# Kernel tuning notes

Measured on AMD Instinct MI355X. Metric: run time of the kernel, lower is better.

The kernel has to match this reference:

```python
import jax, jax.numpy as jnp
import numpy as np

NEG = -1e20
EPS = float(np.finfo(np.float32).eps)


def setup_inputs() -> dict:
    key = jax.random.key(0)
    k1, k2, k3, k4 = jax.random.split(key, 4)
    B, S, E, D = 8, 2048, 1024, 1024
    return {
        "embeddings": jax.random.normal(k1, (B, S, E), dtype=jnp.float32),
        "mask": jnp.ones((B, S), dtype=jnp.int32),
        "W_q": jax.random.normal(k2, (E, D), dtype=jnp.float32),
        "W_k": jax.random.normal(k3, (E, D), dtype=jnp.float32),
        "W_v": jax.random.normal(k4, (E, D), dtype=jnp.float32),
    }


def reference(embeddings, mask, W_q, W_k, W_v):
    # embeddings: [B,S,E]; mask: [B,S] (1 = keep, 0 = pad)
    q = embeddings @ W_q            # [B,S,D]
    k = embeddings @ W_k            # [B,S,D]
    v = embeddings @ W_v            # [B,S,Dv]
    energy = jnp.einsum("bqd,bkd->bqk", q, k)  # [B,S,S]
    S = embeddings.shape[1]
    causal = jnp.tril(jnp.ones((S, S), dtype=bool))          # [S,S]
    energy = jnp.where(causal[None, :, :], energy, NEG)
    pad = (mask == 0)[:, None, :]                             # [B,1,S]
    energy = jnp.where(pad, NEG, energy)
    d_k = jnp.float32(W_k.shape[1])
    scale = jnp.sqrt(d_k) + EPS
    attention = jax.nn.softmax(energy / scale, axis=-1)       # [B,S,S]
    output = jnp.einsum("bqk,bkd->bqd", attention, v)         # [B,S,Dv]
    return output, attention
```

## Files before the change

kernel.cpp:

```cpp
#include <hip/hip_runtime.h>

#define Bb 8
#define Ss 2048
#define Ee 1024
#define Dd 1024

typedef __attribute__((ext_vector_type(8))) __bf16 bf16x8;
typedef __attribute__((ext_vector_type(4))) float f32x4;
typedef unsigned short u16;

__device__ __forceinline__ u16 f2bf(float x) {
  unsigned u = __float_as_uint(x);
  return (u16)((u + 0x7fffu + ((u >> 16) & 1u)) >> 16);
}
__device__ __forceinline__ float bf2f(u16 h) {
  return __uint_as_float(((unsigned)h) << 16);
}

__device__ __forceinline__ void gload16(const void* g, void* l) {
  __builtin_amdgcn_global_load_lds(
      (__attribute__((address_space(1))) void*)const_cast<void*>(g),
      (__attribute__((address_space(3))) void*)l, 16, 0, 0);
}

#define MFMA_BF16 __builtin_amdgcn_mfma_f32_16x16x32_bf16

__global__ __launch_bounds__(256) void k_split4(const float* __restrict__ in,
                                                u16* __restrict__ hi,
                                                u16* __restrict__ lo,
                                                long long n4) {
  long long i = (long long)blockIdx.x * 256 + threadIdx.x;
  if (i >= n4) return;
  float4 v = ((const float4*)in)[i];
  float xs[4] = {v.x, v.y, v.z, v.w};
  u16 hh[4], ll[4];
#pragma unroll
  for (int j = 0; j < 4; ++j) {
    hh[j] = f2bf(xs[j]);
    ll[j] = f2bf(xs[j] - bf2f(hh[j]));
  }
  ushort4 h, l;
  h.x = hh[0]; h.y = hh[1]; h.z = hh[2]; h.w = hh[3];
  l.x = ll[0]; l.y = ll[1]; l.z = ll[2]; l.w = ll[3];
  ((ushort4*)hi)[i] = h;
  ((ushort4*)lo)[i] = l;
}

__global__ __launch_bounds__(256) void k_wt_split(const float* __restrict__ W,
                                                  u16* __restrict__ hi,
                                                  u16* __restrict__ lo) {
  __shared__ float t[32][33];
  const int tx = threadIdx.x & 31;
  const int ty = threadIdx.x >> 5;
  const int e0 = blockIdx.y * 32, d0 = blockIdx.x * 32;
#pragma unroll
  for (int r = ty; r < 32; r += 8)
    t[r][tx] = W[(long long)(e0 + r) * Dd + d0 + tx];
  __syncthreads();
#pragma unroll
  for (int r = ty; r < 32; r += 8) {
    float x = t[tx][r];
    long long o = (long long)(d0 + r) * Ee + e0 + tx;
    u16 h = f2bf(x);
    hi[o] = h;
    if (lo) lo[o] = f2bf(x - bf2f(h));
  }
}

template <int NP, int EPI, bool CAUSAL, bool TRIK>
__global__ __launch_bounds__(512, 4) void k_t128(
    const u16* __restrict__ Ah, const u16* __restrict__ Al,
    const u16* __restrict__ Bh, const u16* __restrict__ Bl,
    float* __restrict__ Cf, u16* __restrict__ Ch, u16* __restrict__ Cl,
    int nbx, int N, int K, long long strA, long long strB, long long strC) {
  constexpr int NMAT = (NP == 3) ? 4 : 2;
  const int nwg = gridDim.x;
  const int f = blockIdx.x;
  const int wgid = (f & 7) * (nwg >> 3) + (f >> 3);
  int bx, by, bz;
  if (CAUSAL) {
    bz = wgid / 136;
    const int t = wgid % 136;
    int yy = 0, c = 0;
    while (c + yy + 1 <= t) { c += yy + 1; ++yy; }
    by = yy;
    bx = t - c;
  } else {
    bz = blockIdx.y;
    bx = wgid % nbx;
    by = wgid / nbx;
  }

  __shared__ __align__(16) u16 lds[2][NMAT][4096];

  const int tid = threadIdx.x;
  const int lane = tid & 63;
  const int w = tid >> 6;
  const int wr = w >> 1;
  const int wc = w & 1;

  const u16* srcBase[NMAT];
  if constexpr (NP == 3) {
    srcBase[0] = Ah + (long long)bz * strA;
    srcBase[1] = Al + (long long)bz * strA;
    srcBase[2] = Bh + (long long)bz * strB;
    srcBase[3] = Bl + (long long)bz * strB;
  } else {
    srcBase[0] = Ah + (long long)bz * strA;
    srcBase[1] = Bh + (long long)bz * strB;
  }
  const long long row0[2] = {(long long)by * 128, (long long)bx * 128};

  const int rL = tid >> 2;
  const int colOff = ((tid & 3) ^ ((tid >> 3) & 3)) * 8;
  const int rdOff = (lane & 15) * 64 + ((((lane >> 4) & 3) ^ ((lane >> 1) & 3)) << 4);

  const int AR = wr * 32;
  const int BR = wc * 64;
  int nt = K / 32;
  if (TRIK) {
    const int lim = ((by + 1) * 128) / 32;
    if (lim < nt) nt = lim;
  }

  const u16* gp[NMAT];
#pragma unroll
  for (int m = 0; m < NMAT; ++m) {
    const int opsel = (NP == 3) ? (m >> 1) : m;
    gp[m] = srcBase[m] + (row0[opsel] + rL) * (long long)K + colOff;
  }

#define STG(BUF)                                                       \
  {                                                                    \
    _Pragma("unroll") for (int m = 0; m < NMAT; ++m) {                 \
      gload16(gp[m], (char*)&lds[BUF][m][0] + tid * 16);               \
      gp[m] += 32;                                                     \
    }                                                                  \
  }
#define LDFRAG(MAT, R) \
  (*(const bf16x8*)((const char*)&lds[cur][MAT][0] + (R)*64 + rdOff))
#define BAR __builtin_amdgcn_s_barrier()

#define CLUSTER3(NH)                                                         \
  __builtin_amdgcn_s_setprio(1);                                             \
  _Pragma("unroll") for (int m = 0; m < 2; ++m)                              \
      _Pragma("unroll") for (int n = 0; n < 2; ++n)                          \
          acc[m][(NH)*2 + n] =                                               \
      MFMA_BF16(aH[m], bL[n], acc[m][(NH)*2 + n], 0, 0, 0);                  \
  _Pragma("unroll") for (int m = 0; m < 2; ++m)                              \
      _Pragma("unroll") for (int n = 0; n < 2; ++n)                          \
          acc[m][(NH)*2 + n] =                                               \
      MFMA_BF16(aL[m], bH[n], acc[m][(NH)*2 + n], 0, 0, 0);                  \
  _Pragma("unroll") for (int m = 0; m < 2; ++m)                              \
      _Pragma("unroll") for (int n = 0; n < 2; ++n)                          \
          acc[m][(NH)*2 + n] =                                               \
      MFMA_BF16(aH[m], bH[n], acc[m][(NH)*2 + n], 0, 0, 0);                  \
  __builtin_amdgcn_s_setprio(0);

  f32x4 acc[2][4];
#pragma unroll
  for (int m = 0; m < 2; ++m)
#pragma unroll
    for (int n = 0; n < 4; ++n) acc[m][n] = f32x4{0.f, 0.f, 0.f, 0.f};

  bf16x8 aH[2], aL[2], bH[2], bL[2];
  bf16x8 bF[4];

  STG(0);

  for (int kt = 0; kt < nt; ++kt) {
    const int cur = kt & 1;
    const bool more = (kt + 1 < nt);

    if (more) {
      STG(cur ^ 1);
      if constexpr (NP == 3)
        asm volatile("s_waitcnt vmcnt(4)" ::: "memory");
      else
        asm volatile("s_waitcnt vmcnt(2)" ::: "memory");
    } else {
      asm volatile("s_waitcnt vmcnt(0)" ::: "memory");
    }
    BAR;

    if constexpr (NP == 3) {
#pragma unroll
      for (int m = 0; m < 2; ++m) {
        aH[m] = LDFRAG(0, AR + m * 16);
        aL[m] = LDFRAG(1, AR + m * 16);
      }
#pragma unroll
      for (int n = 0; n < 2; ++n) {
        bH[n] = LDFRAG(2, BR + n * 16);
        bL[n] = LDFRAG(3, BR + n * 16);
      }
      BAR;
      CLUSTER3(0);
      BAR;
#pragma unroll
      for (int n = 0; n < 2; ++n) {
        bH[n] = LDFRAG(2, BR + 32 + n * 16);
        bL[n] = LDFRAG(3, BR + 32 + n * 16);
      }
      BAR;
      CLUSTER3(1);
      BAR;
    } else {
#pragma unroll
      for (int m = 0; m < 2; ++m) aH[m] = LDFRAG(0, AR + m * 16);
#pragma unroll
      for (int n = 0; n < 4; ++n) bF[n] = LDFRAG(1, BR + n * 16);
      BAR;
      __builtin_amdgcn_s_setprio(1);
#pragma unroll
      for (int m = 0; m < 2; ++m)
#pragma unroll
        for (int n = 0; n < 4; ++n)
          acc[m][n] = MFMA_BF16(aH[m], bF[n], acc[m][n], 0, 0, 0);
      __builtin_amdgcn_s_setprio(0);
      BAR;
    }
  }

  const int cr = (lane >> 4) << 2;
  const int cc = lane & 15;
#pragma unroll
  for (int m = 0; m < 2; ++m)
#pragma unroll
    for (int n = 0; n < 4; ++n)
#pragma unroll
      for (int r = 0; r < 4; ++r) {
        const long long row = (long long)by * 128 + wr * 32 + m * 16 + cr + r;
        const long long col = (long long)bx * 128 + wc * 64 + n * 16 + cc;
        const float v = acc[m][n][r];
        if constexpr (EPI == 0) {
          Cf[(long long)bz * strC + row * N + col] = v;
        } else if constexpr (EPI == 1) {
          const long long idx = row * N + col;
          u16 h = f2bf(v);
          Ch[idx] = h;
          Cl[idx] = f2bf(v - bf2f(h));
        } else {
          Ch[(long long)bz * strC + row * N + col] = f2bf(v);
        }
      }
#undef STG
#undef LDFRAG
#undef BAR
#undef CLUSTER3
}

template <int EPI>
__global__ __launch_bounds__(512, 4) void k_s256(
    const u16* __restrict__ Ah, const u16* __restrict__ Al,
    const u16* __restrict__ Bh, const u16* __restrict__ Bl,
    float* __restrict__ Cf, u16* __restrict__ Ch, u16* __restrict__ Cl,
    int nbx, int N, int K) {
  constexpr int OFF_AL = 16384;
  constexpr int OFF_BH = 32768;
  constexpr int OFF_BL = 40960;
  __shared__ __align__(16) char lds[49152];

  const int nwg = gridDim.x;
  const int f = blockIdx.x;
  const int wgid = (f & 7) * (nwg >> 3) + (f >> 3);
  const int bx = wgid % nbx;
  const int by = wgid / nbx;

  const int tid = threadIdx.x;
  const int lane = tid & 63;
  const int w = tid >> 6;
  const int wr = w >> 1;
  const int wc = w & 1;
  const int AR = wr * 64;
  const int BR = wc * 64;

  const int rL = tid >> 2;
  const int colOff = ((tid & 3) ^ ((tid >> 3) & 3)) * 8;
  const int rdOff = (lane & 15) * 64 + ((((lane >> 4) & 3) ^ ((lane >> 1) & 3)) << 4);

  const long long rowA0 = (long long)by * 256;
  const long long rowB0 = (long long)bx * 128;
  const int nt = K / 32;

  const u16* gp[6];
  int dst[6];
  gp[0] = Ah + (rowA0 + rL) * (long long)K + colOff;        dst[0] = tid * 16;
  gp[1] = Ah + (rowA0 + 128 + rL) * (long long)K + colOff;  dst[1] = 8192 + tid * 16;
  gp[2] = Al + (rowA0 + rL) * (long long)K + colOff;        dst[2] = OFF_AL + tid * 16;
  gp[3] = Al + (rowA0 + 128 + rL) * (long long)K + colOff;  dst[3] = OFF_AL + 8192 + tid * 16;
  gp[4] = Bh + (rowB0 + rL) * (long long)K + colOff;        dst[4] = OFF_BH + tid * 16;
  gp[5] = Bl + (rowB0 + rL) * (long long)K + colOff;        dst[5] = OFF_BL + tid * 16;

  f32x4 acc[4][4];
#pragma unroll
  for (int m = 0; m < 4; ++m)
#pragma unroll
    for (int n = 0; n < 4; ++n) acc[m][n] = f32x4{0.f, 0.f, 0.f, 0.f};

  for (int kt = 0; kt < nt; ++kt) {
#pragma unroll
    for (int u = 0; u < 6; ++u) {
      gload16(gp[u], lds + dst[u]);
      gp[u] += 32;
    }
    asm volatile("s_waitcnt vmcnt(0)" ::: "memory");
    __builtin_amdgcn_s_barrier();

    bf16x8 aH[4], aL[4];
#pragma unroll
    for (int m = 0; m < 4; ++m) {
      aH[m] = *(const bf16x8*)(lds + (AR + m * 16) * 64 + rdOff);
      aL[m] = *(const bf16x8*)(lds + OFF_AL + (AR + m * 16) * 64 + rdOff);
    }
#pragma unroll
    for (int n = 0; n < 4; ++n) {
      bf16x8 bH = *(const bf16x8*)(lds + OFF_BH + (BR + n * 16) * 64 + rdOff);
      bf16x8 bL = *(const bf16x8*)(lds + OFF_BL + (BR + n * 16) * 64 + rdOff);
#pragma unroll
      for (int m = 0; m < 4; ++m)
        acc[m][n] = MFMA_BF16(aH[m], bL, acc[m][n], 0, 0, 0);
#pragma unroll
      for (int m = 0; m < 4; ++m)
        acc[m][n] = MFMA_BF16(aL[m], bH, acc[m][n], 0, 0, 0);
#pragma unroll
      for (int m = 0; m < 4; ++m)
        acc[m][n] = MFMA_BF16(aH[m], bH, acc[m][n], 0, 0, 0);
    }
    __builtin_amdgcn_s_barrier();
  }

  const int cr = (lane >> 4) << 2;
  const int cc = lane & 15;
#pragma unroll
  for (int m = 0; m < 4; ++m)
#pragma unroll
    for (int n = 0; n < 4; ++n)
#pragma unroll
      for (int r = 0; r < 4; ++r) {
        const long long row = (long long)by * 256 + AR + m * 16 + cr + r;
        const long long col = (long long)bx * 128 + BR + n * 16 + cc;
        const float v = acc[m][n][r];
        if constexpr (EPI == 0) {
          Cf[row * N + col] = v;
        } else {
          const long long idx = row * N + col;
          u16 h = f2bf(v);
          Ch[idx] = h;
          Cl[idx] = f2bf(v - bf2f(h));
        }
      }
}

template <int EPI, bool TRIK>
__global__ __launch_bounds__(512, 4) void k_t256(
    const u16* __restrict__ Ah, const u16* __restrict__ Bh,
    float* __restrict__ Cf, u16* __restrict__ Ch,
    int nbx, int N, int K, long long strA, long long strB, long long strC) {
  constexpr int OFF_BH = 16384;
  __shared__ __align__(16) char lds[2][24576];

  const int nwg = gridDim.x;
  const int f = blockIdx.x;
  const int wgid = (f & 7) * (nwg >> 3) + (f >> 3);
  const int bz = blockIdx.y;
  const int bx = wgid % nbx;
  const int by = wgid / nbx;

  const int tid = threadIdx.x;
  const int lane = tid & 63;
  const int w = tid >> 6;
  const int wr = w >> 1;
  const int wc = w & 1;
  const int AR = wr * 64;
  const int BR = wc * 64;

  const int rL = tid >> 2;
  const int colOff = ((tid & 3) ^ ((tid >> 3) & 3)) * 8;
  const int rdOff = (lane & 15) * 64 + ((((lane >> 4) & 3) ^ ((lane >> 1) & 3)) << 4);

  const long long rowA0 = (long long)by * 256;
  const long long rowB0 = (long long)bx * 128;

  int nt = K / 32;
  if (TRIK) {
    const int lim = (by + 1) * 8;
    if (lim < nt) nt = lim;
  }

  const u16* pA = Ah + (long long)bz * strA;
  const u16* pB = Bh + (long long)bz * strB;
  const u16* gp[3];
  int dst[3];
  gp[0] = pA + (rowA0 + rL) * (long long)K + colOff;        dst[0] = tid * 16;
  gp[1] = pA + (rowA0 + 128 + rL) * (long long)K + colOff;  dst[1] = 8192 + tid * 16;
  gp[2] = pB + (rowB0 + rL) * (long long)K + colOff;        dst[2] = OFF_BH + tid * 16;

#define STG(BUF)                                               \
  {                                                            \
    _Pragma("unroll") for (int u = 0; u < 3; ++u) {            \
      gload16(gp[u], lds[BUF] + dst[u]);                       \
      gp[u] += 32;                                             \
    }                                                          \
  }
#define BAR __builtin_amdgcn_s_barrier()

  f32x4 acc[4][4];
#pragma unroll
  for (int m = 0; m < 4; ++m)
#pragma unroll
    for (int n = 0; n < 4; ++n) acc[m][n] = f32x4{0.f, 0.f, 0.f, 0.f};

  STG(0);

  for (int kt = 0; kt < nt; ++kt) {
    const int cur = kt & 1;
    const bool more = (kt + 1 < nt);

    if (more) {
      STG(cur ^ 1);
      asm volatile("s_waitcnt vmcnt(3)" ::: "memory");
    } else {
      asm volatile("s_waitcnt vmcnt(0)" ::: "memory");
    }
    BAR;

    const char* bb = lds[cur];
    bf16x8 a[4], b[4];
#pragma unroll
    for (int m = 0; m < 4; ++m)
      a[m] = *(const bf16x8*)(bb + (AR + m * 16) * 64 + rdOff);
#pragma unroll
    for (int n = 0; n < 4; ++n)
      b[n] = *(const bf16x8*)(bb + OFF_BH + (BR + n * 16) * 64 + rdOff);
#pragma unroll
    for (int m = 0; m < 4; ++m)
#pragma unroll
      for (int n = 0; n < 4; ++n)
        acc[m][n] = MFMA_BF16(a[m], b[n], acc[m][n], 0, 0, 0);
    BAR;
  }

  const int cr = (lane >> 4) << 2;
  const int cc = lane & 15;
#pragma unroll
  for (int m = 0; m < 4; ++m)
#pragma unroll
    for (int n = 0; n < 4; ++n)
#pragma unroll
      for (int r = 0; r < 4; ++r) {
        const long long row = (long long)by * 256 + AR + m * 16 + cr + r;
        const long long col = (long long)bx * 128 + BR + n * 16 + cc;
        const float v = acc[m][n][r];
        if constexpr (EPI == 0) {
          Cf[(long long)bz * strC + row * N + col] = v;
        } else {
          Ch[(long long)bz * strC + row * N + col] = f2bf(v);
        }
      }
#undef STG
#undef BAR
}

__global__ __launch_bounds__(256) void k_softmax(float* __restrict__ attn,
                                                 u16* __restrict__ attn_bf,
                                                 const int* __restrict__ mask,
                                                 float inv_scale) {
  const int q = blockIdx.x;
  const int b = blockIdx.y;
  const int tid = threadIdx.x;
  float* row = attn + ((long long)b * Ss + q) * Ss;
  u16* rowb = attn_bf + ((long long)b * Ss + q) * Ss;
  const int* mrow = mask + b * Ss;
  const int qup = ((q >> 8) + 1) << 8;

  float x[8];
  float m = -3.0e38f;
#pragma unroll
  for (int j = 0; j < 8; ++j) {
    const int k = tid + j * 256;
    float v = -3.0e38f;
    if (k <= q) {
      const float e = row[k];
      v = ((mrow[k] != 0) ? e : -1e20f) * inv_scale;
    }
    x[j] = v;
    m = fmaxf(m, v);
  }
#pragma unroll
  for (int o = 32; o > 0; o >>= 1) m = fmaxf(m, __shfl_xor(m, o));
  __shared__ float redm[4], reds[4];
  const int w = tid >> 6;
  if ((tid & 63) == 0) redm[w] = m;
  __syncthreads();
  m = fmaxf(fmaxf(redm[0], redm[1]), fmaxf(redm[2], redm[3]));
  float s = 0.f;
#pragma unroll
  for (int j = 0; j < 8; ++j) {
    x[j] = __expf(x[j] - m);
    s += x[j];
  }
#pragma unroll
  for (int o = 32; o > 0; o >>= 1) s += __shfl_xor(s, o);
  if ((tid & 63) == 0) reds[w] = s;
  __syncthreads();
  s = reds[0] + reds[1] + reds[2] + reds[3];
  const float inv = 1.0f / s;
#pragma unroll
  for (int j = 0; j < 8; ++j) {
    const int k = tid + j * 256;
    if (k <= q) {
      const float a = x[j] * inv;
      row[k] = a;
      rowb[k] = f2bf(a);
    } else {
      row[k] = 0.0f;
      if (k < qup) rowb[k] = 0;
    }
  }
}

extern "C" void kernel_launch(void* const* d_in, const int* in_sizes, int n_in,
                              void* d_out, int out_size, void* d_ws, size_t ws_size,
                              hipStream_t stream) {
  const float* emb = (const float*)d_in[0];
  const int* mask = (const int*)d_in[1];
  const float* Wq = (const float*)d_in[2];
  const float* Wk = (const float*)d_in[3];
  const float* Wv = (const float*)d_in[4];

  float* out = (float*)d_out;
  float* attn = out + (long long)Bb * Ss * Dd;

  char* p = (char*)d_ws;
  u16* emb_hi = (u16*)p;
  u16* emb_lo = emb_hi + 16777216LL;
  u16* R_hi = (u16*)(p + 67108864LL);
  u16* R_lo = R_hi + 16777216LL;
  u16* v_t = R_lo + 16777216LL;
  u16* attn_bf = v_t + 16777216LL;
  u16* Wqr_hi = attn_bf + 16777216LL;
  u16* Wqr_lo = Wqr_hi + 1048576LL;
  u16* Wkr_hi = Wqr_lo + 1048576LL;
  u16* Wkr_lo = Wkr_hi + 1048576LL;
  u16* M_hi = Wkr_lo + 1048576LL;
  u16* M_lo = M_hi + 1048576LL;
  u16* WvT_hi = M_lo + 1048576LL;

  const float inv_scale = 1.0f / (32.0f + 1.1920929e-07f);

  k_split4<<<16384, 256, 0, stream>>>(emb, emb_hi, emb_lo, 4194304LL);
  k_split4<<<1024, 256, 0, stream>>>(Wq, Wqr_hi, Wqr_lo, 262144LL);
  k_split4<<<1024, 256, 0, stream>>>(Wk, Wkr_hi, Wkr_lo, 262144LL);
  k_wt_split<<<dim3(32, 32), 256, 0, stream>>>(Wv, WvT_hi, nullptr);

  k_t128<3, 1, false, false><<<64, 512, 0, stream>>>(
      Wkr_hi, Wkr_lo, Wqr_hi, Wqr_lo, nullptr, M_hi, M_lo,
      8, 1024, 1024, 0, 0, 0);
  k_s256<1><<<512, 512, 0, stream>>>(
      emb_hi, emb_lo, M_hi, M_lo, nullptr, R_hi, R_lo, 8, 1024, 1024);
  k_t256<2, false><<<dim3(64, 8), 512, 0, stream>>>(
      WvT_hi, emb_hi, nullptr, v_t,
      16, Ss, Ee, 0, (long long)Ss * Ee, (long long)Dd * Ss);
  k_t128<3, 0, true, false><<<1088, 512, 0, stream>>>(
      R_hi, R_lo, emb_hi, emb_lo, attn, nullptr, nullptr,
      0, Ss, Dd, (long long)Ss * Dd, (long long)Ss * Dd, (long long)Ss * Ss);
  k_softmax<<<dim3(Ss, Bb), 256, 0, stream>>>(attn, attn_bf, mask, inv_scale);
  k_t256<0, true><<<dim3(64, 8), 512, 0, stream>>>(
      attn_bf, v_t, out, nullptr,
      8, Dd, Ss, (long long)Ss * Ss, (long long)Dd * Ss, (long long)Ss * Dd);
}
```

Baseline: 449.6 us.

## Replace PV GEMM with 128x128-tile causal kernel using longest-first scheduling

Replaces the 256x128-tile attention·V GEMM (512 workgroups of 512 threads) with a dedicated 128x128-tile kernel (1024 workgroups of 256 threads). The new kernel truncates the K loop at the causal diagonal at 128-row granularity and orders row blocks from the bottom of the matrix first, so the longest tiles start earliest. The softmax now zero-fills its bf16 output only up to the next 128-column boundary to match. The aim is less wasted causal work and better load balance across CUs, at the cost of smaller tiles with less data reuse per loaded byte.

```diff
diff --git a/kernel.cpp b/kernel.cpp
--- a/kernel.cpp
+++ b/kernel.cpp
@@ -67,7 +67,7 @@
   }
 }
 
-template <int NP, int EPI, bool CAUSAL, bool TRIK>
+template <int NP, int EPI, bool CAUSAL>
 __global__ __launch_bounds__(512, 4) void k_t128(
     const u16* __restrict__ Ah, const u16* __restrict__ Al,
     const u16* __restrict__ Bh, const u16* __restrict__ Bl,
@@ -117,11 +117,7 @@
 
   const int AR = wr * 32;
   const int BR = wc * 64;
-  int nt = K / 32;
-  if (TRIK) {
-    const int lim = ((by + 1) * 128) / 32;
-    if (lim < nt) nt = lim;
-  }
+  const int nt = K / 32;
 
   const u16* gp[NMAT];
 #pragma unroll
@@ -352,7 +348,7 @@
       }
 }
 
-template <int EPI, bool TRIK>
+template <int EPI>
 __global__ __launch_bounds__(512, 4) void k_t256(
     const u16* __restrict__ Ah, const u16* __restrict__ Bh,
     float* __restrict__ Cf, u16* __restrict__ Ch,
@@ -381,12 +377,7 @@
 
   const long long rowA0 = (long long)by * 256;
   const long long rowB0 = (long long)bx * 128;
-
-  int nt = K / 32;
-  if (TRIK) {
-    const int lim = (by + 1) * 8;
-    if (lim < nt) nt = lim;
-  }
+  const int nt = K / 32;
 
   const u16* pA = Ah + (long long)bz * strA;
   const u16* pB = Bh + (long long)bz * strB;
@@ -462,6 +453,107 @@
 #undef BAR
 }
 
+__global__ __launch_bounds__(256, 4) void k_pv128(
+    const u16* __restrict__ A, const u16* __restrict__ B,
+    float* __restrict__ C) {
+  __shared__ __align__(16) u16 lds[2][2][4096];
+
+  const int f = blockIdx.x;
+  const int wgid = (f & 7) * 128 + (f >> 3);
+  const int bz = wgid >> 7;
+  const int t = wgid & 127;
+  const int by = 15 - (t >> 3);
+  const int bx = t & 7;
+
+  const int tid = threadIdx.x;
+  const int lane = tid & 63;
+  const int w = tid >> 6;
+  const int wr = w >> 1;
+  const int wc = w & 1;
+  const int AR = wr * 64;
+  const int BR = wc * 64;
+
+  const int rL = tid >> 2;
+  const int colOff = ((tid & 3) ^ ((tid >> 3) & 3)) * 8;
+  const int rdOff = (lane & 15) * 64 + ((((lane >> 4) & 3) ^ ((lane >> 1) & 3)) << 4);
+
+  const int nt = (by + 1) * 4;
+
+  const u16* pA = A + (long long)bz * Ss * Ss;
+  const u16* pB = B + (long long)bz * Dd * Ss;
+  const long long rowA0 = (long long)by * 128;
+  const long long rowB0 = (long long)bx * 128;
+
+  const u16* gp[4];
+  int dst[4];
+  gp[0] = pA + (rowA0 + rL) * (long long)Ss + colOff;       dst[0] = tid * 16;
+  gp[1] = pA + (rowA0 + 64 + rL) * (long long)Ss + colOff;  dst[1] = 4096 + tid * 16;
+  gp[2] = pB + (rowB0 + rL) * (long long)Ss + colOff;       dst[2] = 8192 + tid * 16;
+  gp[3] = pB + (rowB0 + 64 + rL) * (long long)Ss + colOff;  dst[3] = 12288 + tid * 16;
+
+#define STG(BUF)                                               \
+  {                                                            \
+    _Pragma("unroll") for (int u = 0; u < 4; ++u) {            \
+      gload16(gp[u], (char*)&lds[BUF][0][0] + dst[u]);         \
+      gp[u] += 32;                                             \
+    }                                                          \
+  }
+#define BAR __builtin_amdgcn_s_barrier()
+
+  f32x4 acc[4][4];
+#pragma unroll
+  for (int m = 0; m < 4; ++m)
+#pragma unroll
+    for (int n = 0; n < 4; ++n) acc[m][n] = f32x4{0.f, 0.f, 0.f, 0.f};
+
+  STG(0);
+
+  for (int kt = 0; kt < nt; ++kt) {
+    const int cur = kt & 1;
+    const bool more = (kt + 1 < nt);
+
+    if (more) {
+      STG(cur ^ 1);
+      asm volatile("s_waitcnt vmcnt(4)" ::: "memory");
+    } else {
+      asm volatile("s_waitcnt vmcnt(0)" ::: "memory");
+    }
+    BAR;
+
+    const char* bb = (const char*)&lds[cur][0][0];
+    bf16x8 a[4], b[4];
+#pragma unroll
+    for (int m = 0; m < 4; ++m)
+      a[m] = *(const bf16x8*)(bb + (AR + m * 16) * 64 + rdOff);
+#pragma unroll
+    for (int n = 0; n < 4; ++n)
+      b[n] = *(const bf16x8*)(bb + 8192 + (BR + n * 16) * 64 + rdOff);
+    __builtin_amdgcn_s_setprio(1);
+#pragma unroll
+    for (int m = 0; m < 4; ++m)
+#pragma unroll
+      for (int n = 0; n < 4; ++n)
+        acc[m][n] = MFMA_BF16(a[m], b[n], acc[m][n], 0, 0, 0);
+    __builtin_amdgcn_s_setprio(0);
+    BAR;
+  }
+
+  const int cr = (lane >> 4) << 2;
+  const int cc = lane & 15;
+#pragma unroll
+  for (int m = 0; m < 4; ++m)
+#pragma unroll
+    for (int n = 0; n < 4; ++n)
+#pragma unroll
+      for (int r = 0; r < 4; ++r) {
+        const long long row = (long long)by * 128 + AR + m * 16 + cr + r;
+        const long long col = (long long)bx * 128 + BR + n * 16 + cc;
+        C[(long long)bz * Ss * Dd + row * Dd + col] = acc[m][n][r];
+      }
+#undef STG
+#undef BAR
+}
+
 __global__ __launch_bounds__(256) void k_softmax(float* __restrict__ attn,
                                                  u16* __restrict__ attn_bf,
                                                  const int* __restrict__ mask,
@@ -472,7 +564,7 @@
   float* row = attn + ((long long)b * Ss + q) * Ss;
   u16* rowb = attn_bf + ((long long)b * Ss + q) * Ss;
   const int* mrow = mask + b * Ss;
-  const int qup = ((q >> 8) + 1) << 8;
+  const int qup = ((q >> 7) + 1) << 7;
 
   float x[8];
   float m = -3.0e38f;
@@ -554,19 +646,17 @@
   k_split4<<<1024, 256, 0, stream>>>(Wk, Wkr_hi, Wkr_lo, 262144LL);
   k_wt_split<<<dim3(32, 32), 256, 0, stream>>>(Wv, WvT_hi, nullptr);
 
-  k_t128<3, 1, false, false><<<64, 512, 0, stream>>>(
+  k_t128<3, 1, false><<<64, 512, 0, stream>>>(
       Wkr_hi, Wkr_lo, Wqr_hi, Wqr_lo, nullptr, M_hi, M_lo,
       8, 1024, 1024, 0, 0, 0);
   k_s256<1><<<512, 512, 0, stream>>>(
       emb_hi, emb_lo, M_hi, M_lo, nullptr, R_hi, R_lo, 8, 1024, 1024);
-  k_t256<2, false><<<dim3(64, 8), 512, 0, stream>>>(
+  k_t256<2><<<dim3(64, 8), 512, 0, stream>>>(
       WvT_hi, emb_hi, nullptr, v_t,
       16, Ss, Ee, 0, (long long)Ss * Ee, (long long)Dd * Ss);
-  k_t128<3, 0, true, false><<<1088, 512, 0, stream>>>(
+  k_t128<3, 0, true><<<1088, 512, 0, stream>>>(
       R_hi, R_lo, emb_hi, emb_lo, attn, nullptr, nullptr,
       0, Ss, Dd, (long long)Ss * Dd, (long long)Ss * Dd, (long long)Ss * Ss);
   k_softmax<<<dim3(Ss, Bb), 256, 0, stream>>>(attn, attn_bf, mask, inv_scale);
-  k_t256<0, true><<<dim3(64, 8), 512, 0, stream>>>(
-      attn_bf, v_t, out, nullptr,
-      8, Dd, Ss, (long long)Ss * Ss, (long long)Dd * Ss, (long long)Ss * Dd);
-}
+  k_pv128<<<1024, 256, 0, stream>>>(attn_bf, v_t, out);
+}
```

Result: faster. 426.6 us (-5.1%).
